# Optimization experiments

Measured on AMD Instinct MI355X. Metric: run time of the kernel, lower is better.

## Reference

```python
import jax, jax.numpy as jnp
import numpy as np
from jax import lax

B_SZ, SEQ, D_MODEL = 8, 2048, 1024
N_LAYER = 2
D_INNER = 2 * D_MODEL          # expand=2
D_STATE = 16
D_CONV = 4
DT_RANK = D_MODEL // 16        # ceil(1024/16)=64
EPS = 1e-5


def setup_inputs() -> dict:
    key = jax.random.key(0)
    ks = jax.random.split(key, 8)
    f = lambda k, shp, sc: jax.random.normal(k, shp, jnp.float32) * sc
    A_log = jnp.tile(jnp.log(jnp.arange(1, D_STATE + 1, dtype=jnp.float32)),
                     (N_LAYER, D_INNER, 1))  # S4D-real init, [L, d_inner, d_state]
    return {
        "x": f(ks[0], (B_SZ, SEQ, D_MODEL), 1.0),
        "in_proj_w": f(ks[1], (N_LAYER, 2 * D_INNER, D_MODEL), 0.02),
        "conv_w": f(ks[2], (N_LAYER, D_INNER, D_CONV), 0.2),
        "conv_b": jnp.zeros((N_LAYER, D_INNER), jnp.float32),
        "x_proj_w": f(ks[3], (N_LAYER, DT_RANK + 2 * D_STATE, D_INNER), 0.02),
        "dt_proj_w": f(ks[4], (N_LAYER, D_INNER, DT_RANK), 0.1),
        "dt_proj_b": f(ks[5], (N_LAYER, D_INNER), 0.5) - 4.0,  # softplus -> small dt
        "A_log": A_log,
        "D_param": jnp.ones((N_LAYER, D_INNER), jnp.float32),
        "out_proj_w": f(ks[6], (N_LAYER, D_MODEL, D_INNER), 0.02),
        "norm_w": jnp.ones((N_LAYER, D_MODEL), jnp.float32),
        "norm_b": jnp.zeros((N_LAYER, D_MODEL), jnp.float32),
    }


def _layer_norm(x, w, b):
    mu = jnp.mean(x, axis=-1, keepdims=True)
    var = jnp.mean(jnp.square(x - mu), axis=-1, keepdims=True)
    return (x - mu) * lax.rsqrt(var + EPS) * w + b


def _causal_dw_conv(x, w, b):
    # x: [B, Lq, d_inner], w: [d_inner, d_conv] depthwise causal conv
    xp = jnp.pad(x, ((0, 0), (D_CONV - 1, 0), (0, 0)))
    L = x.shape[1]
    y = b
    for k in range(D_CONV):
        y = y + xp[:, k:k + L, :] * w[:, k]
    return y


def _selective_scan(u, dt, Bm, Cm, A, Dp):
    # u, dt: [B, Lq, d_inner]; Bm, Cm: [B, Lq, d_state]; A: [d_inner, d_state]
    def step(h, inp):
        ut, dtt, Bt, Ct = inp                         # [B,di],[B,di],[B,ds],[B,ds]
        dA = jnp.exp(dtt[..., None] * A)              # [B, di, ds]
        h = dA * h + (dtt * ut)[..., None] * Bt[:, None, :]
        y = jnp.einsum('bds,bs->bd', h, Ct)
        return h, y

    h0 = jnp.zeros((u.shape[0], D_INNER, D_STATE), u.dtype)
    xs = (u.transpose(1, 0, 2), dt.transpose(1, 0, 2),
          Bm.transpose(1, 0, 2), Cm.transpose(1, 0, 2))
    _, ys = lax.scan(step, h0, xs)                    # ys: [Lq, B, di]
    return ys.transpose(1, 0, 2) + u * Dp


def _mamba(x, in_w, cw, cb, xpw, dtw, dtb, A_log, Dp, ow):
    xz = jnp.einsum('bld,ed->ble', x, in_w)           # [B, L, 2*d_inner]
    xi, z = jnp.split(xz, 2, axis=-1)
    xc = jax.nn.silu(_causal_dw_conv(xi, cw, cb))     # [B, L, d_inner]
    xdbl = jnp.einsum('bld,ed->ble', xc, xpw)         # [B, L, dt_rank+2*d_state]
    dt_low = xdbl[..., :DT_RANK]
    Bm = xdbl[..., DT_RANK:DT_RANK + D_STATE]
    Cm = xdbl[..., DT_RANK + D_STATE:]
    dt = jax.nn.softplus(jnp.einsum('blr,dr->bld', dt_low, dtw) + dtb)
    A = -jnp.exp(A_log)                               # [d_inner, d_state]
    y = _selective_scan(xc, dt, Bm, Cm, A, Dp)
    y = y * jax.nn.silu(z)
    return jnp.einsum('ble,de->bld', y, ow)           # [B, L, d_model]


def reference(x, in_proj_w, conv_w, conv_b, x_proj_w, dt_proj_w, dt_proj_b,
              A_log, D_param, out_proj_w, norm_w, norm_b):
    residual = None
    for l in range(N_LAYER):
        residual = x if residual is None else x + residual
        h = _layer_norm(residual, norm_w[l], norm_b[l])
        x = _mamba(h, in_proj_w[l], conv_w[l], conv_b[l], x_proj_w[l],
                   dt_proj_w[l], dt_proj_b[l], A_log[l], D_param[l], out_proj_w[l])
    # NOTE: source forward returns x without applying norm_f
    return x
```

## Files before the change

### kernel.cpp

```cpp
#include <hip/hip_runtime.h>
#include <cstddef>
#include <cstdint>

#define SEQB   8
#define SEQL   2048
#define DMODEL 1024
#define DINNER 2048
#define DSTATE 16
#define NC     32
#define TC     64
#define TT     8

typedef __attribute__((ext_vector_type(4))) float f32x4;
typedef __attribute__((ext_vector_type(8))) short bf16x8;
typedef unsigned int u32;
typedef const __attribute__((address_space(1))) u32* gas_ptr;
typedef __attribute__((address_space(3))) u32* las_ptr;

__device__ __forceinline__ void gld16(const void* g, void* l){
  __builtin_amdgcn_global_load_lds((gas_ptr)g, (las_ptr)l, 16, 0, 0);
}

__device__ __forceinline__ float siluf(float x){ return x / (1.f + __expf(-x)); }
__device__ __forceinline__ float softplusf(float x){ return (x > 20.f) ? x : log1pf(__expf(x)); }

__device__ __forceinline__ unsigned short f2bf_rne(float f){
  unsigned int u = __float_as_uint(f);
  u += 0x7FFFu + ((u>>16)&1u);
  return (unsigned short)(u>>16);
}
__device__ __forceinline__ void split_bf(float f, unsigned short& h, unsigned short& l){
  unsigned short hs = f2bf_rne(f);
  float hf = __uint_as_float(((unsigned int)hs)<<16);
  h = hs;
  l = f2bf_rne(f - hf);
}

__global__ __launch_bounds__(256)
void wsplit2(const float* __restrict__ src, unsigned short* __restrict__ dst,
             int K, int k4shift)
{
  int idx = blockIdx.x*256 + threadIdx.x;
  int r  = idx >> k4shift;
  int c4 = idx & ((1<<k4shift)-1);
  float4 v = ((const float4*)src)[idx];
  unsigned short h,l; short4 h4, l4;
  split_bf(v.x,h,l); h4.x=(short)h; l4.x=(short)l;
  split_bf(v.y,h,l); h4.y=(short)h; l4.y=(short)l;
  split_bf(v.z,h,l); h4.z=(short)h; l4.z=(short)l;
  split_bf(v.w,h,l); h4.w=(short)h; l4.w=(short)l;
  size_t ro = (size_t)r*2*K;
  *(short4*)&dst[ro + (c4<<2)]     = h4;
  *(short4*)&dst[ro + K + (c4<<2)] = l4;
}

__global__ __launch_bounds__(256)
void wsplit_og(const float* __restrict__ src, unsigned short* __restrict__ dst)
{
  int idx = blockIdx.x*256 + threadIdx.x;
  int r  = idx >> 9;
  int c4 = idx & 511;
  int layer = r >> 10, rr = r & 1023;
  float4 v = ((const float4*)src)[idx];
  unsigned short h,l; short4 h4, l4;
  split_bf(v.x,h,l); h4.x=(short)h; l4.x=(short)l;
  split_bf(v.y,h,l); h4.y=(short)h; l4.y=(short)l;
  split_bf(v.z,h,l); h4.z=(short)h; l4.z=(short)l;
  split_bf(v.w,h,l); h4.w=(short)h; l4.w=(short)l;
  int col = c4 << 2;
  int g = col >> 8, j = col & 255;
  size_t base = (size_t)layer*1024*4096 + (size_t)rr*4096 + g*512 + j;
  *(short4*)&dst[base]       = h4;
  *(short4*)&dst[base + 256] = l4;
}

__global__ __launch_bounds__(256)
void ln_split2(const float* __restrict__ a, const float* __restrict__ res,
               const float* __restrict__ w, const float* __restrict__ bias,
               unsigned short* __restrict__ Hs)
{
  int row = blockIdx.x;
  size_t off = (size_t)row * DMODEL;
  float4 v = ((const float4*)(a + off))[threadIdx.x];
  if (res){
    float4 u = ((const float4*)(res + off))[threadIdx.x];
    v.x += u.x; v.y += u.y; v.z += u.z; v.w += u.w;
  }
  float s  = v.x + v.y + v.z + v.w;
  float s2 = fmaf(v.x,v.x, fmaf(v.y,v.y, fmaf(v.z,v.z, v.w*v.w)));
  #pragma unroll
  for (int o=32;o>0;o>>=1){ s += __shfl_down(s,o,64); s2 += __shfl_down(s2,o,64); }
  __shared__ float red[8];
  int lane = threadIdx.x & 63, wid = threadIdx.x >> 6;
  if (lane==0){ red[wid]=s; red[4+wid]=s2; }
  __syncthreads();
  s  = red[0]+red[1]+red[2]+red[3];
  s2 = red[4]+red[5]+red[6]+red[7];
  float mu  = s * (1.f/DMODEL);
  float var = s2 * (1.f/DMODEL) - mu*mu;
  float rstd = rsqrtf(var + 1e-5f);
  float4 wv = ((const float4*)w)[threadIdx.x];
  float4 bv = ((const float4*)bias)[threadIdx.x];
  float4 o4;
  o4.x = (v.x-mu)*rstd*wv.x + bv.x;
  o4.y = (v.y-mu)*rstd*wv.y + bv.y;
  o4.z = (v.z-mu)*rstd*wv.z + bv.z;
  o4.w = (v.w-mu)*rstd*wv.w + bv.w;
  unsigned short h,l; short4 h4, l4;
  split_bf(o4.x,h,l); h4.x=(short)h; l4.x=(short)l;
  split_bf(o4.y,h,l); h4.y=(short)h; l4.y=(short)l;
  split_bf(o4.z,h,l); h4.z=(short)h; l4.z=(short)l;
  split_bf(o4.w,h,l); h4.w=(short)h; l4.w=(short)l;
  size_t ro = (size_t)row*2048;
  int c = threadIdx.x<<2;
  *(short4*)&Hs[ro + c]        = h4;
  *(short4*)&Hs[ro + 1024 + c] = l4;
}

__global__ __launch_bounds__(256)
void mgemm_in(const unsigned short* __restrict__ A,
              const unsigned short* __restrict__ B,
              float* __restrict__ XI, float* __restrict__ ZB)
{
  __shared__ __align__(16) unsigned short As[128*64];
  __shared__ __align__(16) unsigned short Bs[128*64];
  const int t = threadIdx.x;
  const int nbx = 32;
  const int total = nbx * gridDim.y;
  const int wg = blockIdx.y * nbx + blockIdx.x;
  const int swz = (wg & 7) * (total >> 3) + (wg >> 3);
  const int mbase = (swz / nbx) << 7;
  const int nbase = (swz % nbx) << 7;

  const int lane = t & 63, w = t >> 6;
  const int wr = w >> 1, wc = w & 1;
  const int l16 = lane & 15, kq = lane >> 4;

  const int sr8 = lane >> 3, sl8 = lane & 7;
  const unsigned short* pA[4]; const unsigned short* pB[4];
  unsigned short* dA[4]; unsigned short* dB[4];
  #pragma unroll
  for (int c=0;c<4;c++){
    int row = c*32 + w*8 + sr8;
    int col = (sl8 ^ (row & 7)) << 3;
    pA[c] = A + (size_t)(mbase+row)*2048 + col;
    pB[c] = B + (size_t)(nbase+row)*2048 + col;
    dA[c] = &As[row*64 + sl8*8];
    dB[c] = &Bs[row*64 + sl8*8];
  }

  f32x4 acc[4][4];
  #pragma unroll
  for (int i=0;i<4;i++)
    #pragma unroll
    for (int j=0;j<4;j++) acc[i][j] = (f32x4){0.f,0.f,0.f,0.f};

  #pragma unroll
  for (int kb=0; kb<3; kb++){
    const int ao = (kb==2) ? 1024 : 0;
    const int bo = (kb==1) ? 1024 : 0;
    for (int kk=0; kk<1024; kk+=64){
      #pragma unroll
      for (int c=0;c<4;c++){
        gld16(pA[c] + ao + kk, dA[c]);
        gld16(pB[c] + bo + kk, dB[c]);
      }
      __syncthreads();
      #pragma unroll
      for (int ks=0; ks<2; ks++){
        const int kcol = kq + ks*4;
        bf16x8 af[4];
        #pragma unroll
        for (int mf=0; mf<4; mf++){
          int ra = wr*64 + mf*16 + l16;
          af[mf] = *(const bf16x8*)&As[ra*64 + ((kcol ^ (ra&7))<<3)];
        }
        #pragma unroll
        for (int nf=0; nf<4; nf++){
          int rb = wc*64 + nf*16 + l16;
          bf16x8 bfr = *(const bf16x8*)&Bs[rb*64 + ((kcol ^ (rb&7))<<3)];
          #pragma unroll
          for (int mf=0; mf<4; mf++)
            acc[mf][nf] = __builtin_amdgcn_mfma_f32_16x16x32_bf16(af[mf], bfr, acc[mf][nf], 0,0,0);
        }
      }
      __syncthreads();
    }
  }

  float* Cd = (nbase < 2048) ? XI : ZB;
  const int cb = (nbase < 2048) ? nbase : (nbase - 2048);
  #pragma unroll
  for (int mf=0; mf<4; mf++){
    int r0 = mbase + wr*64 + mf*16 + kq*4;
    #pragma unroll
    for (int nf=0; nf<4; nf++){
      int c = cb + wc*64 + nf*16 + l16;
      #pragma unroll
      for (int r=0;r<4;r++)
        Cd[(size_t)(r0+r)*2048 + c] = acc[mf][nf][r];
    }
  }
}

__global__ __launch_bounds__(256)
void mgemm_out3(const unsigned short* __restrict__ A,
                const unsigned short* __restrict__ B,
                float* __restrict__ C)
{
  __shared__ __align__(16) unsigned short As[128*64];
  __shared__ __align__(16) unsigned short Bs[128*64];
  const int t = threadIdx.x;
  const int nbx = 8;
  const int total = nbx * gridDim.y;
  const int wg = blockIdx.y * nbx + blockIdx.x;
  const int swz = (wg & 7) * (total >> 3) + (wg >> 3);
  const int mbase = (swz / nbx) << 7;
  const int nbase = (swz % nbx) << 7;

  const int lane = t & 63, w = t >> 6;
  const int wr = w >> 1, wc = w & 1;
  const int l16 = lane & 15, kq = lane >> 4;

  const int sr8 = lane >> 3, sl8 = lane & 7;
  const unsigned short* pA[4]; const unsigned short* pB[4];
  unsigned short* dA[4]; unsigned short* dB[4];
  #pragma unroll
  for (int c=0;c<4;c++){
    int row = c*32 + w*8 + sr8;
    int col = (sl8 ^ (row & 7)) << 3;
    pA[c] = A + (size_t)(mbase+row)*4096 + col;
    pB[c] = B + (size_t)(nbase+row)*4096 + col;
    dA[c] = &As[row*64 + sl8*8];
    dB[c] = &Bs[row*64 + sl8*8];
  }

  f32x4 acc[4][4];
  #pragma unroll
  for (int i=0;i<4;i++)
    #pragma unroll
    for (int j=0;j<4;j++) acc[i][j] = (f32x4){0.f,0.f,0.f,0.f};

  #pragma unroll
  for (int kb=0; kb<3; kb++){
    const int pa_ = (kb==2) ? 256 : 0;
    const int pb_ = (kb==1) ? 256 : 0;
    for (int v=0; v<2048; v+=64){
      const int gso = ((v>>8)<<9) + (v & 255);
      #pragma unroll
      for (int c=0;c<4;c++){
        gld16(pA[c] + gso + pa_, dA[c]);
        gld16(pB[c] + gso + pb_, dB[c]);
      }
      __syncthreads();
      #pragma unroll
      for (int ks=0; ks<2; ks++){
        const int kcol = kq + ks*4;
        bf16x8 af[4];
        #pragma unroll
        for (int mf=0; mf<4; mf++){
          int ra = wr*64 + mf*16 + l16;
          af[mf] = *(const bf16x8*)&As[ra*64 + ((kcol ^ (ra&7))<<3)];
        }
        #pragma unroll
        for (int nf=0; nf<4; nf++){
          int rb = wc*64 + nf*16 + l16;
          bf16x8 bfr = *(const bf16x8*)&Bs[rb*64 + ((kcol ^ (rb&7))<<3)];
          #pragma unroll
          for (int mf=0; mf<4; mf++)
            acc[mf][nf] = __builtin_amdgcn_mfma_f32_16x16x32_bf16(af[mf], bfr, acc[mf][nf], 0,0,0);
        }
      }
      __syncthreads();
    }
  }

  #pragma unroll
  for (int mf=0; mf<4; mf++){
    int r0 = mbase + wr*64 + mf*16 + kq*4;
    #pragma unroll
    for (int nf=0; nf<4; nf++){
      int c = nbase + wc*64 + nf*16 + l16;
      #pragma unroll
      for (int r=0;r<4;r++)
        C[(size_t)(r0+r)*1024 + c] = acc[mf][nf][r];
    }
  }
}

__global__ __launch_bounds__(256)
void xproj_pair(const unsigned short* __restrict__ A,
                const unsigned short* __restrict__ W2,
                float* __restrict__ XD)
{
  __shared__ __align__(16) unsigned short As_[32*32];
  __shared__ __align__(16) unsigned short Bs_[96*32];
  const int t = threadIdx.x;
  const int mbase = blockIdx.x << 5;
  const int lane = t & 63, w = t >> 6;
  const int mf = w & 1, nc0 = (w >> 1) * 48;
  const int l16 = lane & 15, kq = lane >> 4;

  const bool isA0 = (w < 2);
  const int rr = lane >> 2, sl = lane & 3;
  const int r0_ = (isA0 ? 16*w : 16*(w-2)) + rr;
  const int sw0 = ((sl ^ ((r0_>>1)&3)) << 3);
  const unsigned short* base0 = isA0 ? (A + (size_t)(mbase+r0_)*4096 + sw0)
                                     : (W2 + (size_t)r0_*4096 + sw0);
  unsigned short* dst0 = isA0 ? (As_ + w*512 + lane*8)
                              : (Bs_ + (w-2)*512 + lane*8);
  const int r1_ = 16*(w+2) + rr;
  const int sw1 = ((sl ^ ((r1_>>1)&3)) << 3);
  const unsigned short* base1 = W2 + (size_t)r1_*4096 + sw1;
  unsigned short* dst1 = Bs_ + (w+2)*512 + lane*8;

  f32x4 acc[3];
  #pragma unroll
  for (int j=0;j<3;j++) acc[j] = (f32x4){0.f,0.f,0.f,0.f};

  #pragma unroll
  for (int kb=0; kb<3; kb++){
    const int ao = (kb==2) ? 2048 : 0;
    const int bo = (kb==1) ? 2048 : 0;
    const int off0 = isA0 ? ao : bo;
    for (int v=0; v<2048; v+=32){
      gld16(base0 + off0 + v, dst0);
      gld16(base1 + bo + v, dst1);
      __syncthreads();
      int ra = mf*16 + l16;
      bf16x8 a = *(const bf16x8*)&As_[ra*32 + ((kq ^ ((ra>>1)&3))<<3)];
      #pragma unroll
      for (int nf=0; nf<3; nf++){
        int rb = nc0 + nf*16 + l16;
        bf16x8 b = *(const bf16x8*)&Bs_[rb*32 + ((kq ^ ((rb>>1)&3))<<3)];
        acc[nf] = __builtin_amdgcn_mfma_f32_16x16x32_bf16(a, b, acc[nf], 0,0,0);
      }
      __syncthreads();
    }
  }
  #pragma unroll
  for (int nf=0; nf<3; nf++){
    int c = nc0 + nf*16 + l16;
    int r0s = mbase + mf*16 + kq*4;
    #pragma unroll
    for (int r=0;r<4;r++)
      XD[(size_t)(r0s+r)*96 + c] = acc[nf][r];
  }
}

__global__ __launch_bounds__(256)
void gemm_dt(const float* __restrict__ A, int lda,
             const float* __restrict__ B, int ldb,
             float* __restrict__ C, int ldc,
             int K, const float* __restrict__ ebias)
{
  __shared__ float As[16][132];
  __shared__ float Bs[16][132];
  int tid = threadIdx.x;
  int tx = tid & 15, ty = tid >> 4;
  int mbase = blockIdx.y << 7;
  int nbase = blockIdx.x << 7;
  float acc[8][8];
  #pragma unroll
  for (int i=0;i<8;i++)
    #pragma unroll
    for (int j=0;j<8;j++) acc[i][j]=0.f;

  for (int k0=0;k0<K;k0+=16){
    #pragma unroll
    for (int it=0; it<2; it++){
      int idx = tid + (it<<8);
      int row = idx >> 2;
      int kq  = (idx & 3) << 2;
      float4 va = *(const float4*)(A + (size_t)(mbase+row)*lda + k0 + kq);
      As[kq+0][row]=va.x; As[kq+1][row]=va.y; As[kq+2][row]=va.z; As[kq+3][row]=va.w;
      float4 vb = *(const float4*)(B + (size_t)(nbase+row)*ldb + k0 + kq);
      Bs[kq+0][row]=vb.x; Bs[kq+1][row]=vb.y; Bs[kq+2][row]=vb.z; Bs[kq+3][row]=vb.w;
    }
    __syncthreads();
    #pragma unroll
    for (int k=0;k<16;k++){
      float a[8], bb[8];
      *(float4*)&a[0]  = *(const float4*)&As[k][ty<<2];
      *(float4*)&a[4]  = *(const float4*)&As[k][64+(ty<<2)];
      *(float4*)&bb[0] = *(const float4*)&Bs[k][tx<<2];
      *(float4*)&bb[4] = *(const float4*)&Bs[k][64+(tx<<2)];
      #pragma unroll
      for (int i=0;i<8;i++)
        #pragma unroll
        for (int j=0;j<8;j++)
          acc[i][j] = fmaf(a[i], bb[j], acc[i][j]);
    }
    __syncthreads();
  }

  int n0 = nbase + (tx<<2);
  int n1 = n0 + 64;
  float4 eb0 = *(const float4*)(ebias + n0);
  float4 eb1 = *(const float4*)(ebias + n1);
  #pragma unroll
  for (int i=0;i<8;i++){
    int mrow = mbase + ((i<4) ? ((ty<<2)+i) : (64 + (ty<<2) + (i-4)));
    float4 c0 = make_float4(acc[i][0],acc[i][1],acc[i][2],acc[i][3]);
    float4 c1 = make_float4(acc[i][4],acc[i][5],acc[i][6],acc[i][7]);
    c0.x = softplusf(c0.x+eb0.x); c0.y = softplusf(c0.y+eb0.y);
    c0.z = softplusf(c0.z+eb0.z); c0.w = softplusf(c0.w+eb0.w);
    c1.x = softplusf(c1.x+eb1.x); c1.y = softplusf(c1.y+eb1.y);
    c1.z = softplusf(c1.z+eb1.z); c1.w = softplusf(c1.w+eb1.w);
    *(float4*)(C + (size_t)mrow*ldc + n0) = c0;
    *(float4*)(C + (size_t)mrow*ldc + n1) = c1;
  }
}

__global__ __launch_bounds__(256)
void conv_silu_kernel(const float* __restrict__ xi, const float* __restrict__ cw,
                      const float* __restrict__ cb, unsigned short* __restrict__ u2)
{
  int idx = blockIdx.x*256 + threadIdx.x;
  int d = idx & (DINNER-1);
  int g = idx >> 11;
  int t0 = (g & 511) << 2;
  int b = g >> 9;
  float4 w4 = *(const float4*)(cw + d*4);
  float bias = cb[d];
  const float* base = xi + (size_t)b*SEQL*DINNER + d;
  float v[7];
  #pragma unroll
  for (int j=0;j<7;j++){
    int t = t0-3+j;
    v[j] = (t>=0) ? base[(size_t)t*DINNER] : 0.f;
  }
  unsigned short* outp = u2 + ((size_t)b*SEQL + t0)*4096 + d;
  #pragma unroll
  for (int j=0;j<4;j++){
    float y = fmaf(v[j+3], w4.w, fmaf(v[j+2], w4.z, fmaf(v[j+1], w4.y, fmaf(v[j], w4.x, bias))));
    float uv = siluf(y);
    unsigned short h,l;
    split_bf(uv, h, l);
    outp[(size_t)j*4096]        = h;
    outp[(size_t)j*4096 + 2048] = l;
  }
}

template<int PASS>
__global__ __launch_bounds__(256)
void scan_chunk(const unsigned short* __restrict__ u2, float* __restrict__ dty,
                const float* __restrict__ xdbl, const float* __restrict__ zb,
                const float* __restrict__ A_log, const float* __restrict__ Dp,
                float* __restrict__ hfin, float* __restrict__ sumdt)
{
  __shared__ __align__(16) float Tdt[TT][256];
  __shared__ __align__(16) float Tu [TT][256];
  __shared__ __align__(16) float Tz [TT][256];

  const int tid = threadIdx.x;
  const int idx = blockIdx.x*256 + tid;
  const int d = idx & (DINNER-1);
  const int g = idx >> 11;
  const int cck = g & (NC-1);
  const int bb = g >> 5;
  const int wv = tid >> 6, ln = tid & 63;
  const int dbase = (blockIdx.x << 8) & (DINNER-1);

  float A2[16];
  {
    const float* al = A_log + (size_t)d*DSTATE;
    #pragma unroll
    for (int s=0;s<16;s++) A2[s] = -expf(al[s]) * 1.44269504f;
  }
  float h[16];
  if (PASS == 1){
    #pragma unroll
    for (int s=0;s<16;s++) h[s] = 0.f;
  } else {
    const float* hp = hfin + ((size_t)g*DINNER + d)*16;
    #pragma unroll
    for (int s=0;s<16;s+=4) *(float4*)&h[s] = *(const float4*)(hp + s);
  }
  const float Dv = (PASS==3) ? Dp[d] : 0.f;

  const size_t row0 = (size_t)bb*SEQL + (size_t)cck*TC;
  const float* pbc = xdbl + row0*96 + 64;

  float Bb[2][16], Cb[2][16];
#define LOAD_BC(buf, t) { const float4* p4 = (const float4*)(pbc + (size_t)(t)*96); \
    *(float4*)&Bb[buf][0]=p4[0]; *(float4*)&Bb[buf][4]=p4[1]; \
    *(float4*)&Bb[buf][8]=p4[2]; *(float4*)&Bb[buf][12]=p4[3]; \
    if (PASS==3){ \
    *(float4*)&Cb[buf][0]=p4[4]; *(float4*)&Cb[buf][4]=p4[5]; \
    *(float4*)&Cb[buf][8]=p4[6]; *(float4*)&Cb[buf][12]=p4[7]; } }

  LOAD_BC(0, 0);
  float sdt = 0.f;

  for (int t0 = 0; t0 < TC; t0 += TT){
    #pragma unroll
    for (int q=0;q<2;q++){
      int r = q*4 + wv;
      size_t rowi = row0 + t0 + r;
      gld16(dty + rowi*2048 + dbase + ln*4, &Tdt[r][0]);
      const unsigned short* us = u2 + rowi*4096 +
          ((ln < 32) ? (dbase + ln*8) : (2048 + dbase + (ln-32)*8));
      gld16(us, &Tu[r][0]);
      if (PASS==3) gld16(zb + rowi*2048 + dbase + ln*4, &Tz[r][0]);
    }
    __syncthreads();

    #pragma unroll
    for (int tt=0; tt<TT; tt++){
      const int t = t0 + tt;
      const int cur = tt & 1, nxt = cur^1;
      float dtc = Tdt[tt][tid];
      const unsigned short* tur = (const unsigned short*)&Tu[tt][0];
      float uc = __uint_as_float((u32)tur[tid] << 16)
               + __uint_as_float((u32)tur[256+tid] << 16);
      float zc  = (PASS==3) ? Tz[tt][tid] : 0.f;
      if (t+1 < TC) LOAD_BC(nxt, t+1);
      if (PASS==1) sdt += dtc;
      float du = dtc*uc;
      float y = 0.f;
      #pragma unroll
      for (int s=0;s<16;s++){
        float dA = exp2f(dtc*A2[s]);
        h[s] = fmaf(dA, h[s], du*Bb[cur][s]);
        if (PASS==3) y = fmaf(h[s], Cb[cur][s], y);
      }
      if (PASS==3){
        y = fmaf(uc, Dv, y);
        float gv = y * siluf(zc);
        unsigned short gh, gl;
        split_bf(gv, gh, gl);
        Tdt[tt][tid] = __uint_as_float((u32)gh | ((u32)gl << 16));
      }
    }

    if (PASS==3){
      __syncthreads();
      #pragma unroll
      for (int q=0;q<2;q++){
        int r = q*4 + wv;
        size_t rowi = row0 + t0 + r;
        const u32* T = (const u32*)&Tdt[r][0];
        int o0 = ln*4;
        u32 vals[4];
        if (ln < 32){
          #pragma unroll
          for (int k=0;k<4;k++){
            int i2 = (o0+k)*2;
            vals[k] = (T[i2] & 0xFFFFu) | (T[i2+1] << 16);
          }
        } else {
          #pragma unroll
          for (int k=0;k<4;k++){
            int i2 = (o0+k-128)*2;
            vals[k] = (T[i2] >> 16) | (T[i2+1] & 0xFFFF0000u);
          }
        }
        *(float4*)(dty + rowi*2048 + dbase + o0) = *(const float4*)vals;
      }
    }
    __syncthreads();
  }
#undef LOAD_BC

  if (PASS==1){
    float* hp = hfin + ((size_t)g*DINNER + d)*16;
    #pragma unroll
    for (int s=0;s<16;s+=4) *(float4*)(hp + s) = *(const float4*)&h[s];
    sumdt[(size_t)g*DINNER + d] = sdt;
  }
}

__global__ __launch_bounds__(256)
void scan_prop(const float* __restrict__ A_log, float* __restrict__ hfin,
               const float* __restrict__ sumdt)
{
  int idx = blockIdx.x*256 + threadIdx.x;
  int s = idx & 15;
  int d = (idx >> 4) & (DINNER-1);
  int b = idx >> 15;
  float A2 = -expf(A_log[(size_t)d*DSTATE + s]) * 1.44269504f;
  float H = 0.f;
  size_t hbase = ((size_t)b*NC*DINNER + d)*16 + s;
  size_t sbase = (size_t)b*NC*DINNER + d;
  for (int c=0;c<NC;c++){
    float P   = exp2f(A2 * sumdt[sbase + (size_t)c*DINNER]);
    float tmp = hfin[hbase + (size_t)c*DINNER*16];
    hfin[hbase + (size_t)c*DINNER*16] = H;
    H = fmaf(P, H, tmp);
  }
}

extern "C" void kernel_launch(void* const* d_in, const int* in_sizes, int n_in,
                              void* d_out, int out_size, void* d_ws, size_t ws_size,
                              hipStream_t stream)
{
  const float* x    = (const float*)d_in[0];
  const float* in_w = (const float*)d_in[1];
  const float* cw   = (const float*)d_in[2];
  const float* cb   = (const float*)d_in[3];
  const float* xpw  = (const float*)d_in[4];
  const float* dtw  = (const float*)d_in[5];
  const float* dtb  = (const float*)d_in[6];
  const float* A_log= (const float*)d_in[7];
  const float* Dp   = (const float*)d_in[8];
  const float* ow   = (const float*)d_in[9];
  const float* nw   = (const float*)d_in[10];
  const float* nb   = (const float*)d_in[11];
  float* outF = (float*)d_out;

  const size_t fixedB = 33554432ULL + 16777216ULL + 1572864ULL;
  const size_t perB   = 58720256ULL;
  int NB = 4;
  while (NB > 1 && fixedB + (size_t)NB*perB > ws_size) NB >>= 1;
  const int Mc = NB * SEQL;
  const int nchunk = SEQB / NB;

  unsigned short* INW2  = (unsigned short*)d_ws;
  unsigned short* OUTWG = INW2 + (size_t)2*4096*2048;
  unsigned short* XPW2  = OUTWG + (size_t)2*1024*4096;
  char* dyn = (char*)(XPW2 + (size_t)2*96*4096);

  unsigned short* SH = (unsigned short*)dyn;
  float* XD = (float*)dyn;
  float* HF = (float*)(dyn + (size_t)Mc*384);
  float* SD = (float*)(dyn + (size_t)Mc*2432);
  float* XI = (float*)(dyn + (size_t)Mc*4096);
  float* ZB = XI + (size_t)Mc*2048;
  unsigned short* U2 = (unsigned short*)(ZB + (size_t)Mc*2048);

  wsplit2<<<8192, 256, 0, stream>>>(in_w, INW2, 1024, 8);
  wsplit2<<<384,  256, 0, stream>>>(xpw,  XPW2, 2048, 9);
  wsplit_og<<<4096, 256, 0, stream>>>(ow, OUTWG);

  for (int c = 0; c < nchunk; ++c){
    const size_t rowoff = (size_t)c * Mc;
    const float* xrows = x + rowoff * DMODEL;
    float* X1 = outF + rowoff * DMODEL;

    for (int l = 0; l < 2; ++l){
      const float* Al = A_log + (size_t)l*DINNER*DSTATE;

      ln_split2<<<Mc, 256, 0, stream>>>(
          (l==0) ? xrows : X1, (l==0) ? nullptr : xrows,
          nw + (size_t)l*DMODEL, nb + (size_t)l*DMODEL, SH);

      mgemm_in<<<dim3(32, Mc/128), 256, 0, stream>>>(
          SH, INW2 + (size_t)l*4096*2048, XI, ZB);

      conv_silu_kernel<<<NB*4096, 256, 0, stream>>>(
          XI, cw + (size_t)l*DINNER*4, cb + (size_t)l*DINNER, U2);

      xproj_pair<<<Mc/32, 256, 0, stream>>>(
          U2, XPW2 + (size_t)l*96*4096, XD);

      gemm_dt<<<dim3(16, Mc/128), 256, 0, stream>>>(
          XD, 96, dtw + (size_t)l*DINNER*64, 64, XI, DINNER, 64,
          dtb + (size_t)l*DINNER);

      scan_chunk<1><<<NB*NC*8, 256, 0, stream>>>(
          U2, XI, XD, ZB, Al, Dp + (size_t)l*DINNER, HF, SD);
      scan_prop<<<NB*128, 256, 0, stream>>>(Al, HF, SD);
      scan_chunk<3><<<NB*NC*8, 256, 0, stream>>>(
          U2, XI, XD, ZB, Al, Dp + (size_t)l*DINNER, HF, SD);

      mgemm_out3<<<dim3(8, Mc/128), 256, 0, stream>>>(
          (const unsigned short*)XI, OUTWG + (size_t)l*1024*4096, X1);
    }
  }
}
```

Baseline: 3.604 ms.

## Double-buffer scan staging, vectorize conv kernel, drop GEMM tile swizzle

The scan kernel now double-buffers its per-tile loads into shared memory, prefetching the next 8 timesteps while computing the current ones. B/C vectors are staged through LDS by one wave instead of being loaded per thread from global memory. The gated output goes to a separate buffer, so the dt tile is no longer overwritten. The conv+silu kernel is rewritten to process one row per block with 8 channels per thread and vectorized 16-byte stores. The two MFMA GEMMs drop their workgroup swizzle for plain blockIdx mapping. This uses more LDS and may cost L2 locality in the GEMMs.

```diff
diff --git a/kernel.cpp b/kernel.cpp
--- a/kernel.cpp
+++ b/kernel.cpp
@@ -125,12 +125,7 @@
   __shared__ __align__(16) unsigned short As[128*64];
   __shared__ __align__(16) unsigned short Bs[128*64];
   const int t = threadIdx.x;
-  const int nbx = 32;
-  const int total = nbx * gridDim.y;
-  const int wg = blockIdx.y * nbx + blockIdx.x;
-  const int swz = (wg & 7) * (total >> 3) + (wg >> 3);
-  const int mbase = (swz / nbx) << 7;
-  const int nbase = (swz % nbx) << 7;
+  const int mbase = blockIdx.y << 7, nbase = blockIdx.x << 7;
 
   const int lane = t & 63, w = t >> 6;
   const int wr = w >> 1, wc = w & 1;
@@ -211,12 +206,7 @@
   __shared__ __align__(16) unsigned short As[128*64];
   __shared__ __align__(16) unsigned short Bs[128*64];
   const int t = threadIdx.x;
-  const int nbx = 8;
-  const int total = nbx * gridDim.y;
-  const int wg = blockIdx.y * nbx + blockIdx.x;
-  const int swz = (wg & 7) * (total >> 3) + (wg >> 3);
-  const int mbase = (swz / nbx) << 7;
-  const int nbase = (swz % nbx) << 7;
+  const int mbase = blockIdx.y << 7, nbase = blockIdx.x << 7;
 
   const int lane = t & 63, w = t >> 6;
   const int wr = w >> 1, wc = w & 1;
@@ -416,30 +406,44 @@
 void conv_silu_kernel(const float* __restrict__ xi, const float* __restrict__ cw,
                       const float* __restrict__ cb, unsigned short* __restrict__ u2)
 {
-  int idx = blockIdx.x*256 + threadIdx.x;
-  int d = idx & (DINNER-1);
-  int g = idx >> 11;
-  int t0 = (g & 511) << 2;
-  int b = g >> 9;
-  float4 w4 = *(const float4*)(cw + d*4);
-  float bias = cb[d];
-  const float* base = xi + (size_t)b*SEQL*DINNER + d;
-  float v[7];
-  #pragma unroll
-  for (int j=0;j<7;j++){
-    int t = t0-3+j;
-    v[j] = (t>=0) ? base[(size_t)t*DINNER] : 0.f;
-  }
-  unsigned short* outp = u2 + ((size_t)b*SEQL + t0)*4096 + d;
-  #pragma unroll
-  for (int j=0;j<4;j++){
-    float y = fmaf(v[j+3], w4.w, fmaf(v[j+2], w4.z, fmaf(v[j+1], w4.y, fmaf(v[j], w4.x, bias))));
+  const int row = blockIdx.x;
+  const int d0 = threadIdx.x << 3;
+  const int tt = row & (SEQL-1);
+
+  float wk[4][8];
+  {
+    const float4* cw4 = (const float4*)(cw + (size_t)d0*4);
+    #pragma unroll
+    for (int j=0;j<8;j++){
+      float4 wj = cw4[j];
+      wk[0][j]=wj.x; wk[1][j]=wj.y; wk[2][j]=wj.z; wk[3][j]=wj.w;
+    }
+  }
+  float bias[8];
+  *(float4*)&bias[0] = *(const float4*)(cb + d0);
+  *(float4*)&bias[4] = *(const float4*)(cb + d0 + 4);
+
+  const float* base = xi + (size_t)row*DINNER + d0;
+  float r0[8], r1[8], r2[8], r3[8];
+#define LD8(dst, p) { *(float4*)&dst[0] = ((const float4*)(p))[0]; \
+                      *(float4*)&dst[4] = ((const float4*)(p))[1]; }
+  LD8(r0, base);
+  if (tt>=1){ LD8(r1, base-DINNER); }   else { for(int j=0;j<8;j++) r1[j]=0.f; }
+  if (tt>=2){ LD8(r2, base-2*DINNER); } else { for(int j=0;j<8;j++) r2[j]=0.f; }
+  if (tt>=3){ LD8(r3, base-3*DINNER); } else { for(int j=0;j<8;j++) r3[j]=0.f; }
+#undef LD8
+
+  unsigned short h8[8], l8[8];
+  #pragma unroll
+  for (int j=0;j<8;j++){
+    float y = fmaf(r0[j], wk[3][j], fmaf(r1[j], wk[2][j],
+              fmaf(r2[j], wk[1][j], fmaf(r3[j], wk[0][j], bias[j]))));
     float uv = siluf(y);
-    unsigned short h,l;
-    split_bf(uv, h, l);
-    outp[(size_t)j*4096]        = h;
-    outp[(size_t)j*4096 + 2048] = l;
-  }
+    split_bf(uv, h8[j], l8[j]);
+  }
+  unsigned short* outp = u2 + (size_t)row*4096 + d0;
+  *(uint4*)outp          = *(const uint4*)h8;
+  *(uint4*)(outp + 2048) = *(const uint4*)l8;
 }
 
 template<int PASS>
@@ -449,9 +453,11 @@
                 const float* __restrict__ A_log, const float* __restrict__ Dp,
                 float* __restrict__ hfin, float* __restrict__ sumdt)
 {
-  __shared__ __align__(16) float Tdt[TT][256];
-  __shared__ __align__(16) float Tu [TT][256];
-  __shared__ __align__(16) float Tz [TT][256];
+  __shared__ __align__(16) float Tdt[2][TT][256];
+  __shared__ __align__(16) float Tu [2][TT][256];
+  __shared__ __align__(16) float Tz [(PASS==3)?2:1][TT][256];
+  __shared__ __align__(16) float Tbc[2][TT][32];
+  __shared__ __align__(16) float Tgy[(PASS==3)?TT:1][256];
 
   const int tid = threadIdx.x;
   const int idx = blockIdx.x*256 + tid;
@@ -480,67 +486,71 @@
   const float Dv = (PASS==3) ? Dp[d] : 0.f;
 
   const size_t row0 = (size_t)bb*SEQL + (size_t)cck*TC;
-  const float* pbc = xdbl + row0*96 + 64;
-
-  float Bb[2][16], Cb[2][16];
-#define LOAD_BC(buf, t) { const float4* p4 = (const float4*)(pbc + (size_t)(t)*96); \
-    *(float4*)&Bb[buf][0]=p4[0]; *(float4*)&Bb[buf][4]=p4[1]; \
-    *(float4*)&Bb[buf][8]=p4[2]; *(float4*)&Bb[buf][12]=p4[3]; \
-    if (PASS==3){ \
-    *(float4*)&Cb[buf][0]=p4[4]; *(float4*)&Cb[buf][4]=p4[5]; \
-    *(float4*)&Cb[buf][8]=p4[6]; *(float4*)&Cb[buf][12]=p4[7]; } }
-
-  LOAD_BC(0, 0);
+
+#define STAGE(buf, T0) do { \
+    _Pragma("unroll") \
+    for (int q=0;q<2;q++){ \
+      int r = q*4 + wv; \
+      size_t rowi = row0 + (T0) + r; \
+      gld16(dty + rowi*2048 + dbase + ln*4, &Tdt[buf][r][0]); \
+      const unsigned short* us = u2 + rowi*4096 + \
+          ((ln < 32) ? (dbase + ln*8) : (2048 + dbase + (ln-32)*8)); \
+      gld16(us, &Tu[buf][r][0]); \
+      if (PASS==3) gld16(zb + rowi*2048 + dbase + ln*4, &Tz[buf][r][0]); \
+    } \
+    if (wv == 3){ \
+      gld16(xdbl + (row0 + (T0) + (ln>>3))*96 + 64 + (ln&7)*4, &Tbc[buf][0][0]); \
+    } \
+  } while(0)
+
+  STAGE(0, 0);
+  __syncthreads();
   float sdt = 0.f;
 
   for (int t0 = 0; t0 < TC; t0 += TT){
-    #pragma unroll
-    for (int q=0;q<2;q++){
-      int r = q*4 + wv;
-      size_t rowi = row0 + t0 + r;
-      gld16(dty + rowi*2048 + dbase + ln*4, &Tdt[r][0]);
-      const unsigned short* us = u2 + rowi*4096 +
-          ((ln < 32) ? (dbase + ln*8) : (2048 + dbase + (ln-32)*8));
-      gld16(us, &Tu[r][0]);
-      if (PASS==3) gld16(zb + rowi*2048 + dbase + ln*4, &Tz[r][0]);
-    }
-    __syncthreads();
+    const int cur = (t0 >> 3) & 1, nxt = cur ^ 1;
+    if (t0 + TT < TC) STAGE(nxt, t0 + TT);
 
     #pragma unroll
     for (int tt=0; tt<TT; tt++){
-      const int t = t0 + tt;
-      const int cur = tt & 1, nxt = cur^1;
-      float dtc = Tdt[tt][tid];
-      const unsigned short* tur = (const unsigned short*)&Tu[tt][0];
+      float dtc = Tdt[cur][tt][tid];
+      const unsigned short* tur = (const unsigned short*)&Tu[cur][tt][0];
       float uc = __uint_as_float((u32)tur[tid] << 16)
                + __uint_as_float((u32)tur[256+tid] << 16);
-      float zc  = (PASS==3) ? Tz[tt][tid] : 0.f;
-      if (t+1 < TC) LOAD_BC(nxt, t+1);
+      float Bv[16], Cv[16];
+      #pragma unroll
+      for (int q=0;q<4;q++) *(float4*)&Bv[q*4] = *(const float4*)&Tbc[cur][tt][q*4];
+      if (PASS==3){
+        #pragma unroll
+        for (int q=0;q<4;q++) *(float4*)&Cv[q*4] = *(const float4*)&Tbc[cur][tt][16+q*4];
+      }
       if (PASS==1) sdt += dtc;
       float du = dtc*uc;
       float y = 0.f;
       #pragma unroll
       for (int s=0;s<16;s++){
         float dA = exp2f(dtc*A2[s]);
-        h[s] = fmaf(dA, h[s], du*Bb[cur][s]);
-        if (PASS==3) y = fmaf(h[s], Cb[cur][s], y);
+        h[s] = fmaf(dA, h[s], du*Bv[s]);
+        if (PASS==3) y = fmaf(h[s], Cv[s], y);
       }
       if (PASS==3){
+        float zc = Tz[cur][tt][tid];
         y = fmaf(uc, Dv, y);
         float gv = y * siluf(zc);
         unsigned short gh, gl;
         split_bf(gv, gh, gl);
-        Tdt[tt][tid] = __uint_as_float((u32)gh | ((u32)gl << 16));
-      }
-    }
+        Tgy[tt][tid] = __uint_as_float((u32)gh | ((u32)gl << 16));
+      }
+    }
+
+    __syncthreads();
 
     if (PASS==3){
-      __syncthreads();
       #pragma unroll
       for (int q=0;q<2;q++){
         int r = q*4 + wv;
         size_t rowi = row0 + t0 + r;
-        const u32* T = (const u32*)&Tdt[r][0];
+        const u32* T = (const u32*)&Tgy[r][0];
         int o0 = ln*4;
         u32 vals[4];
         if (ln < 32){
@@ -558,10 +568,10 @@
         }
         *(float4*)(dty + rowi*2048 + dbase + o0) = *(const float4*)vals;
       }
-    }
-    __syncthreads();
-  }
-#undef LOAD_BC
+      __syncthreads();
+    }
+  }
+#undef STAGE
 
   if (PASS==1){
     float* hp = hfin + ((size_t)g*DINNER + d)*16;
@@ -648,7 +658,7 @@
       mgemm_in<<<dim3(32, Mc/128), 256, 0, stream>>>(
           SH, INW2 + (size_t)l*4096*2048, XI, ZB);
 
-      conv_silu_kernel<<<NB*4096, 256, 0, stream>>>(
+      conv_silu_kernel<<<Mc, 256, 0, stream>>>(
           XI, cw + (size_t)l*DINNER*4, cb + (size_t)l*DINNER, U2);
 
       xproj_pair<<<Mc/32, 256, 0, stream>>>(
```

Result: slower. 3.794 ms (+5.3%).
